# Optimization experiments

Measured on AMD Instinct MI355X. Metric: run time of the kernel, lower is better.

Reference implementation:

```python
import jax, jax.numpy as jnp
import numpy as np

NUM_EMBEDDINGS = 512
EMBEDDING_DIM = 128
COMMITMENT = 0.25
DECAY = 0.99
EPS = 1e-05


def setup_inputs() -> dict:
    key = jax.random.key(0)
    k1, k2 = jax.random.split(key)
    z = jax.random.normal(k1, (32, EMBEDDING_DIM, 64, 64), dtype=jnp.float32)
    embedding = jax.random.normal(k2, (EMBEDDING_DIM, NUM_EMBEDDINGS), dtype=jnp.float32)
    cluster_size = jnp.zeros((NUM_EMBEDDINGS,), dtype=jnp.float32)
    embed_avg = embedding  # buffer initialized as a clone of embedding
    return {"z": z, "embedding": embedding, "cluster_size": cluster_size, "embed_avg": embed_avg}


def reference(z, embedding, cluster_size, embed_avg):
    sg = jax.lax.stop_gradient
    D, K = embedding.shape
    B, C, H, W = z.shape
    z_perm = jnp.transpose(z, (0, 2, 3, 1))          # [B,H,W,D]
    flat_z = z_perm.reshape(-1, D)                    # [N,D]

    distances = ((flat_z ** 2).sum(1, keepdims=True)
                 - 2.0 * (flat_z @ embedding)
                 + (embedding ** 2).sum(0)[None, :])  # [N,K]
    idx = jnp.argmin(distances, axis=1)               # [N]

    # gather codes (equivalent to one-hot @ embedding.T, without materializing one-hot)
    quantized = jnp.take(embedding.T, idx, axis=0).reshape(z_perm.shape)  # [B,H,W,D]
    quantized = jnp.transpose(quantized, (0, 3, 1, 2))                    # [B,D,H,W]

    # EMA codebook update (training branch)
    enc_sum = jax.ops.segment_sum(jnp.ones_like(idx, dtype=flat_z.dtype), idx, num_segments=K)  # [K]
    embed_sum = jax.ops.segment_sum(flat_z, idx, num_segments=K).T                              # [D,K]
    new_cluster_size = cluster_size * DECAY + (1.0 - DECAY) * enc_sum
    new_embed_avg = embed_avg * DECAY + (1.0 - DECAY) * embed_sum
    n = jnp.maximum(new_cluster_size.sum(), 1e-05)
    cs = (new_cluster_size + EPS) / (n + K * EPS) * n
    new_embedding = new_embed_avg / cs[None, :]

    e_latent_loss = jnp.mean((sg(quantized) - z) ** 2)
    q_latent_loss = jnp.mean((quantized - sg(z)) ** 2)
    loss = q_latent_loss + COMMITMENT * e_latent_loss

    quantized_out = z + sg(quantized - z)             # straight-through
    encoding_indices = idx.reshape(B, H, W)
    return (quantized_out, loss, encoding_indices, new_embedding, new_cluster_size, new_embed_avg)
```

## Files before the change

kernel.cpp:

```cpp
#include <hip/hip_runtime.h>
#include <hip/hip_bf16.h>
#include <float.h>

typedef _Float16 f16;
typedef __attribute__((ext_vector_type(8))) _Float16 half8;
typedef __attribute__((ext_vector_type(4))) float floatx4;

#define DIM   128
#define HW    4096
#define NPOS  131072
#define K     512
#define ZSTRIDE_B 524288

#define Q_OFF     0
#define LOSS_OFF  16777216
#define IDX_OFF   16777217
#define NEMB_OFF  16908289
#define NCS_OFF   16973825
#define NEA_OFF   16974337

#define WS_LOSS  0
#define WS_E2    2
#define WS_ENC   514
#define WS_ESUM  1026
#define WS_ZERO_COUNT 66562
#define WS_EHI   66564
#define WS_ELO   99332

#define XST 136

__global__ __launch_bounds__(256) void k_prep(const float* __restrict__ emb,
                                              f16* __restrict__ ehiP,
                                              f16* __restrict__ eloP,
                                              float* __restrict__ e2) {
    int lin = blockIdx.x * 256 + threadIdx.x;
    int d = lin >> 9, k = lin & 511;
    float v = emb[lin];
    unsafeAtomicAdd(&e2[k], v * v);
    f16 h = (f16)v;
    f16 l = (f16)(v - (float)h);
    int g = k >> 4, r = k & 15;
    int dc = d >> 5, w = d & 31, quad = w >> 3, j = w & 7;
    int idx = (g * 4 + dc) * 512 + quad * 128 + r * 8 + j;
    ehiP[idx] = h;
    eloP[idx] = l;
}

__global__ __launch_bounds__(256, 2) void k_assign(const float* __restrict__ z,
                                                   const f16* __restrict__ ehiP,
                                                   const f16* __restrict__ eloP,
                                                   const float* __restrict__ e2,
                                                   float* __restrict__ out,
                                                   float* __restrict__ lossAcc) {
    __shared__ f16 xs_h[64 * XST];
    __shared__ f16 xs_l[64 * XST];
    __shared__ float wbD[256];
    __shared__ int   wbI[256];
    __shared__ int   bidx[64];
    __shared__ float wred[4];

    const int tid  = threadIdx.x;
    const int lane = tid & 63;
    const int wv   = tid >> 6;
    const int n0   = blockIdx.x * 64;
    const int b    = n0 >> 12;
    const int hw0  = n0 & 4095;
    const float* zb = z + b * ZSTRIDE_B + hw0;
    const int l15  = lane & 15;
    const int quad = lane >> 4;

    float sv0[16], sv1[16];
    #pragma unroll
    for (int it = 0; it < 16; ++it) {
        int lin = tid + it * 256;
        int i  = lin & 63;
        int dp = lin >> 6;
        sv0[it] = zb[(2 * dp) * HW + i];
        sv1[it] = zb[(2 * dp + 1) * HW + i];
    }
    #pragma unroll
    for (int it = 0; it < 16; ++it) {
        int lin = tid + it * 256;
        int i  = lin & 63;
        int dp = lin >> 6;
        float v0 = sv0[it], v1 = sv1[it];
        f16 h0 = (f16)v0; f16 l0 = (f16)(v0 - (float)h0);
        f16 h1 = (f16)v1; f16 l1 = (f16)(v1 - (float)h1);
        union { f16 h[2]; unsigned int u; } ph, pl;
        ph.h[0] = h0; ph.h[1] = h1;
        pl.h[0] = l0; pl.h[1] = l1;
        *(unsigned int*)&xs_h[i * XST + 2 * dp] = ph.u;
        *(unsigned int*)&xs_l[i * XST + 2 * dp] = pl.u;
    }
    __syncthreads();

    float bestD[4][4];
    int   bestI[4][4];
    #pragma unroll
    for (int t = 0; t < 4; ++t)
        #pragma unroll
        for (int r = 0; r < 4; ++r) { bestD[t][r] = FLT_MAX; bestI[t][r] = 0x7fffffff; }

    const half8* gh = (const half8*)ehiP;
    const half8* gl = (const half8*)eloP;

    for (int cc = 0; cc < 4; ++cc) {
        floatx4 acc[4][2];
        #pragma unroll
        for (int t = 0; t < 4; ++t)
            #pragma unroll
            for (int nt = 0; nt < 2; ++nt) acc[t][nt] = (floatx4){0.f, 0.f, 0.f, 0.f};

        for (int dc = 0; dc < 4; ++dc) {
            half8 ah[4], al[4];
            #pragma unroll
            for (int t = 0; t < 4; ++t) {
                int off = (t * 16 + l15) * XST + dc * 32 + quad * 8;
                ah[t] = *(const half8*)&xs_h[off];
                al[t] = *(const half8*)&xs_l[off];
            }
            #pragma unroll
            for (int nt = 0; nt < 2; ++nt) {
                int g  = cc * 8 + wv * 2 + nt;
                int bi = (g * 4 + dc) * 64 + lane;
                half8 bh = gh[bi];
                half8 bl = gl[bi];
                #pragma unroll
                for (int t = 0; t < 4; ++t) {
                    acc[t][nt] = __builtin_amdgcn_mfma_f32_16x16x32_f16(ah[t], bh, acc[t][nt], 0, 0, 0);
                    acc[t][nt] = __builtin_amdgcn_mfma_f32_16x16x32_f16(al[t], bh, acc[t][nt], 0, 0, 0);
                    acc[t][nt] = __builtin_amdgcn_mfma_f32_16x16x32_f16(ah[t], bl, acc[t][nt], 0, 0, 0);
                }
            }
        }
        #pragma unroll
        for (int nt = 0; nt < 2; ++nt) {
            int c = cc * 128 + wv * 32 + nt * 16 + l15;
            float ee = e2[c];
            #pragma unroll
            for (int t = 0; t < 4; ++t)
                #pragma unroll
                for (int r = 0; r < 4; ++r) {
                    float s = fmaf(-2.f, acc[t][nt][r], ee);
                    if (s < bestD[t][r]) { bestD[t][r] = s; bestI[t][r] = c; }
                }
        }
    }

    #pragma unroll
    for (int mask = 1; mask <= 8; mask <<= 1) {
        #pragma unroll
        for (int t = 0; t < 4; ++t)
            #pragma unroll
            for (int r = 0; r < 4; ++r) {
                float od = __shfl_xor(bestD[t][r], mask, 64);
                int   oi = __shfl_xor(bestI[t][r], mask, 64);
                if (od < bestD[t][r] || (od == bestD[t][r] && oi < bestI[t][r])) {
                    bestD[t][r] = od; bestI[t][r] = oi;
                }
            }
    }
    if (l15 == 0) {
        #pragma unroll
        for (int t = 0; t < 4; ++t)
            #pragma unroll
            for (int r = 0; r < 4; ++r) {
                int m = t * 16 + quad * 4 + r;
                wbD[wv * 64 + m] = bestD[t][r];
                wbI[wv * 64 + m] = bestI[t][r];
            }
    }
    __syncthreads();
    if (tid < 64) {
        float bd = wbD[tid]; int bi = wbI[tid];
        #pragma unroll
        for (int w = 1; w < 4; ++w) {
            float od = wbD[w * 64 + tid]; int oi = wbI[w * 64 + tid];
            if (od < bd || (od == bd && oi < bi)) { bd = od; bi = oi; }
        }
        bidx[tid] = bi;
        out[IDX_OFF + n0 + tid] = (float)bi;
    }
    __syncthreads();

    float* qb = out + Q_OFF + b * ZSTRIDE_B + hw0;
    float lsum = 0.f;
    #pragma unroll
    for (int it = 0; it < 4; ++it) {
        int o = wv * 4 + it;
        int c = bidx[lane];
        int g = c >> 4, r = c & 15;
        int base = (g * 4 + (o >> 2)) * 512 + (o & 3) * 128 + r * 8;
        half8 hh = *(const half8*)&ehiP[base];
        half8 ll = *(const half8*)&eloP[base];
        half8 zh = *(const half8*)&xs_h[lane * XST + o * 8];
        half8 zl = *(const half8*)&xs_l[lane * XST + o * 8];
        #pragma unroll
        for (int jj = 0; jj < 8; ++jj) {
            float q  = (float)hh[jj] + (float)ll[jj];
            float zz = (float)zh[jj] + (float)zl[jj];
            qb[(o * 8 + jj) * HW + lane] = q;
            float df = q - zz;
            lsum = fmaf(df, df, lsum);
        }
    }
    #pragma unroll
    for (int m = 32; m >= 1; m >>= 1) lsum += __shfl_xor(lsum, m, 64);
    if (lane == 0) wred[wv] = lsum;
    __syncthreads();
    if (tid == 0) unsafeAtomicAdd(lossAcc, wred[0] + wred[1] + wred[2] + wred[3]);
}

#define DC 8
__global__ __launch_bounds__(256) void k_ema2(const float* __restrict__ z,
                                              const float* __restrict__ out,
                                              float* __restrict__ enc,
                                              float* __restrict__ esum) {
    __shared__ float acc[DC][K];
    __shared__ float cnt[K];

    const int tid = threadIdx.x;
    const int half   = blockIdx.x & 1;
    const int dchunk = (blockIdx.x >> 1) & 15;
    const int b      = blockIdx.x >> 5;
    const int d0 = dchunk * DC;
    const bool doCnt = (dchunk == 0);

    for (int i = tid; i < DC * K; i += 256) ((float*)acc)[i] = 0.f;
    if (doCnt) for (int i = tid; i < K; i += 256) cnt[i] = 0.f;
    __syncthreads();

    const float* zb  = z + b * ZSTRIDE_B;
    const float* idp = out + IDX_OFF + b * HW;

    const int p0 = half * 2048;
    for (int t = p0; t < p0 + 2048; t += 1024) {
        const int p = t + 4 * tid;
        float4 iv = *(const float4*)(idp + p);
        int k0 = (int)iv.x;
        int k1 = (int)iv.y;
        int k2 = (int)iv.z;
        int k3 = (int)iv.w;
        if (doCnt) {
            atomicAdd(&cnt[k0], 1.f); atomicAdd(&cnt[k1], 1.f);
            atomicAdd(&cnt[k2], 1.f); atomicAdd(&cnt[k3], 1.f);
        }
        #pragma unroll
        for (int d = 0; d < DC; ++d) {
            float4 zv = *(const float4*)(zb + (d0 + d) * HW + p);
            atomicAdd(&acc[d][k0], zv.x);
            atomicAdd(&acc[d][k1], zv.y);
            atomicAdd(&acc[d][k2], zv.z);
            atomicAdd(&acc[d][k3], zv.w);
        }
    }
    __syncthreads();

    const int rot = (blockIdx.x & 31) << 6;
    for (int i = tid; i < DC * K; i += 256) {
        int j = (i + rot) & (DC * K - 1);
        int d = j >> 9, k = j & 511;
        unsafeAtomicAdd(&esum[(d0 + d) * K + k], acc[d][k]);
    }
    if (doCnt) for (int i = tid; i < K; i += 256) unsafeAtomicAdd(&enc[i], cnt[i]);
}

__global__ __launch_bounds__(512) void k_final(const float* __restrict__ enc,
                                               const float* __restrict__ cs_in,
                                               const float* __restrict__ lossAcc,
                                               const float* __restrict__ esum,
                                               const float* __restrict__ eavg_in,
                                               float* __restrict__ out) {
    __shared__ float red[512];
    int k = threadIdx.x;
    int d = blockIdx.x;
    float ncs = fmaf(cs_in[k], 0.99f, 0.01f * enc[k]);
    red[k] = ncs;
    __syncthreads();
    for (int s = 256; s > 0; s >>= 1) {
        if (k < s) red[k] += red[k + s];
        __syncthreads();
    }
    float nn = fmaxf(red[0], 1e-5f);
    float cs = (ncs + 1e-5f) / (nn + (float)K * 1e-5f) * nn;
    float ea = fmaf(eavg_in[d * K + k], 0.99f, 0.01f * esum[d * K + k]);
    out[NEA_OFF + d * K + k] = ea;
    out[NEMB_OFF + d * K + k] = ea / cs;
    if (d == 0) {
        out[NCS_OFF + k] = ncs;
        if (k == 0) out[LOSS_OFF] = lossAcc[0] * 1.25f / 16777216.0f;
    }
}

extern "C" void kernel_launch(void* const* d_in, const int* in_sizes, int n_in,
                              void* d_out, int out_size, void* d_ws, size_t ws_size,
                              hipStream_t stream) {
    const float* z     = (const float*)d_in[0];
    const float* emb   = (const float*)d_in[1];
    const float* cs_in = (const float*)d_in[2];
    const float* eavg  = (const float*)d_in[3];
    float* out = (float*)d_out;
    float* wsF = (float*)d_ws;

    hipMemsetAsync(wsF, 0, WS_ZERO_COUNT * sizeof(float), stream);

    k_prep<<<256, 256, 0, stream>>>(emb, (f16*)(wsF + WS_EHI), (f16*)(wsF + WS_ELO),
                                    wsF + WS_E2);
    k_assign<<<NPOS / 64, 256, 0, stream>>>(z,
                                            (const f16*)(wsF + WS_EHI),
                                            (const f16*)(wsF + WS_ELO),
                                            wsF + WS_E2, out, wsF + WS_LOSS);
    k_ema2<<<1024, 256, 0, stream>>>(z, out, wsF + WS_ENC, wsF + WS_ESUM);
    k_final<<<128, 512, 0, stream>>>(wsF + WS_ENC, cs_in, wsF + WS_LOSS,
                                     wsF + WS_ESUM, eavg, out);
}
```

Baseline: 305.8 us.

## Prefetch codebook fragments per chunk and vectorize codebook prep kernel

In the assign kernel, all B-operand (codebook hi/lo) fragments for a 128-code chunk are loaded into registers up front, and the dc loop is fully unrolled so global loads are issued ahead of the MFMA chain. The occupancy hint of 2 blocks per SM is dropped from launch bounds, which frees registers for the prefetched fragments but may reduce occupancy. The prep kernel now has each thread handle 8 dims, writing half8 vectors and issuing one atomic per thread instead of per element, with 8x fewer blocks.

```diff
diff --git a/kernel.cpp b/kernel.cpp
--- a/kernel.cpp
+++ b/kernel.cpp
@@ -34,24 +34,30 @@
                                               f16* __restrict__ eloP,
                                               float* __restrict__ e2) {
     int lin = blockIdx.x * 256 + threadIdx.x;
-    int d = lin >> 9, k = lin & 511;
-    float v = emb[lin];
-    unsafeAtomicAdd(&e2[k], v * v);
-    f16 h = (f16)v;
-    f16 l = (f16)(v - (float)h);
+    int o = lin >> 9, k = lin & 511;
     int g = k >> 4, r = k & 15;
-    int dc = d >> 5, w = d & 31, quad = w >> 3, j = w & 7;
-    int idx = (g * 4 + dc) * 512 + quad * 128 + r * 8 + j;
-    ehiP[idx] = h;
-    eloP[idx] = l;
-}
-
-__global__ __launch_bounds__(256, 2) void k_assign(const float* __restrict__ z,
-                                                   const f16* __restrict__ ehiP,
-                                                   const f16* __restrict__ eloP,
-                                                   const float* __restrict__ e2,
-                                                   float* __restrict__ out,
-                                                   float* __restrict__ lossAcc) {
+    half8 hh, ll;
+    float s = 0.f;
+    #pragma unroll
+    for (int j = 0; j < 8; ++j) {
+        float v = emb[(o * 8 + j) * K + k];
+        f16 h = (f16)v;
+        f16 l = (f16)(v - (float)h);
+        hh[j] = h; ll[j] = l;
+        s = fmaf(v, v, s);
+    }
+    int base = (g * 4 + (o >> 2)) * 512 + (o & 3) * 128 + r * 8;
+    *(half8*)&ehiP[base] = hh;
+    *(half8*)&eloP[base] = ll;
+    unsafeAtomicAdd(&e2[k], s);
+}
+
+__global__ __launch_bounds__(256) void k_assign(const float* __restrict__ z,
+                                                const f16* __restrict__ ehiP,
+                                                const f16* __restrict__ eloP,
+                                                const float* __restrict__ e2,
+                                                float* __restrict__ out,
+                                                float* __restrict__ lossAcc) {
     __shared__ f16 xs_h[64 * XST];
     __shared__ f16 xs_l[64 * XST];
     __shared__ float wbD[256];
@@ -105,12 +111,24 @@
     const half8* gl = (const half8*)eloP;
 
     for (int cc = 0; cc < 4; ++cc) {
+        half8 Bh[4][2], Bl[4][2];
+        #pragma unroll
+        for (int dc = 0; dc < 4; ++dc)
+            #pragma unroll
+            for (int nt = 0; nt < 2; ++nt) {
+                int g  = cc * 8 + wv * 2 + nt;
+                int bi = (g * 4 + dc) * 64 + lane;
+                Bh[dc][nt] = gh[bi];
+                Bl[dc][nt] = gl[bi];
+            }
+
         floatx4 acc[4][2];
         #pragma unroll
         for (int t = 0; t < 4; ++t)
             #pragma unroll
             for (int nt = 0; nt < 2; ++nt) acc[t][nt] = (floatx4){0.f, 0.f, 0.f, 0.f};
 
+        #pragma unroll
         for (int dc = 0; dc < 4; ++dc) {
             half8 ah[4], al[4];
             #pragma unroll
@@ -121,15 +139,11 @@
             }
             #pragma unroll
             for (int nt = 0; nt < 2; ++nt) {
-                int g  = cc * 8 + wv * 2 + nt;
-                int bi = (g * 4 + dc) * 64 + lane;
-                half8 bh = gh[bi];
-                half8 bl = gl[bi];
                 #pragma unroll
                 for (int t = 0; t < 4; ++t) {
-                    acc[t][nt] = __builtin_amdgcn_mfma_f32_16x16x32_f16(ah[t], bh, acc[t][nt], 0, 0, 0);
-                    acc[t][nt] = __builtin_amdgcn_mfma_f32_16x16x32_f16(al[t], bh, acc[t][nt], 0, 0, 0);
-                    acc[t][nt] = __builtin_amdgcn_mfma_f32_16x16x32_f16(ah[t], bl, acc[t][nt], 0, 0, 0);
+                    acc[t][nt] = __builtin_amdgcn_mfma_f32_16x16x32_f16(ah[t], Bh[dc][nt], acc[t][nt], 0, 0, 0);
+                    acc[t][nt] = __builtin_amdgcn_mfma_f32_16x16x32_f16(al[t], Bh[dc][nt], acc[t][nt], 0, 0, 0);
+                    acc[t][nt] = __builtin_amdgcn_mfma_f32_16x16x32_f16(ah[t], Bl[dc][nt], acc[t][nt], 0, 0, 0);
                 }
             }
         }
@@ -304,8 +318,8 @@
 
     hipMemsetAsync(wsF, 0, WS_ZERO_COUNT * sizeof(float), stream);
 
-    k_prep<<<256, 256, 0, stream>>>(emb, (f16*)(wsF + WS_EHI), (f16*)(wsF + WS_ELO),
-                                    wsF + WS_E2);
+    k_prep<<<32, 256, 0, stream>>>(emb, (f16*)(wsF + WS_EHI), (f16*)(wsF + WS_ELO),
+                                   wsF + WS_E2);
     k_assign<<<NPOS / 64, 256, 0, stream>>>(z,
                                             (const f16*)(wsF + WS_EHI),
                                             (const f16*)(wsF + WS_ELO),
```

Result: slower. 348.3 us (+13.9%).
